# Kernel tuning notes

Hardware: AMD Instinct MI355X
Metric: run time of the kernel (lower is better)

## Reference

```python
import jax, jax.numpy as jnp
import numpy as np

B = 8388608  # 2^23 rows -> each [B,4] activation is 128 MB
N_LAYERS = 99


def setup_inputs() -> dict:
    key = jax.random.key(0)
    ks = jax.random.split(key, 7)
    return {
        "x": jax.random.normal(ks[0], (B, 2), dtype=jnp.float32),
        "W_in": jax.random.normal(ks[1], (2, 4), dtype=jnp.float32) * 0.5,
        "b_in": jax.random.normal(ks[2], (4,), dtype=jnp.float32) * 0.1,
        "Ws": jax.random.normal(ks[3], (N_LAYERS, 4, 4), dtype=jnp.float32) * 0.5,
        "bs": jax.random.normal(ks[4], (N_LAYERS, 4), dtype=jnp.float32) * 0.1,
        "W_out": jax.random.normal(ks[5], (4, 1), dtype=jnp.float32) * 0.5,
        "b_out": jax.random.normal(ks[6], (1,), dtype=jnp.float32) * 0.1,
    }


def reference(x, W_in, b_in, Ws, bs, W_out, b_out):
    # input layer + relu
    out = jax.nn.relu(x @ W_in + b_in)  # [B, 4]
    skip = out
    # torch condition `if i % 5 and i != 0` == residual whenever i % 5 != 0
    flags = (jnp.arange(N_LAYERS) % 5) != 0  # [99] bool

    def step(carry, layer):
        out, skip = carry
        W, b, flag = layer  # W: [4,4], b: [4]
        h = jax.nn.relu(out @ W + b)  # Linear(4,4) + ReLU
        new_out = jnp.where(flag, h + skip, h)
        new_skip = jnp.where(flag, new_out, skip)
        return (new_out, new_skip), None

    (out, skip), _ = jax.lax.scan(step, (out, skip), (Ws, bs, flags))
    return out @ W_out + b_out  # [B, 1]
```

## Files before the change

kernel.cpp:

```cpp
#include <hip/hip_runtime.h>


#define NLAYERS 99

__global__ __launch_bounds__(256) void skipmlp_kernel(
    const float* __restrict__ x,
    const float* __restrict__ W_in,
    const float* __restrict__ b_in,
    const float* __restrict__ Ws,
    const float* __restrict__ bs,
    const float* __restrict__ W_out,
    const float* __restrict__ b_out,
    float* __restrict__ out,
    int B)
{
    int row = blockIdx.x * blockDim.x + threadIdx.x;
    if (row >= B) return;

    const float2 xv = *reinterpret_cast<const float2*>(x + (size_t)row * 2u);

    float o0 = fmaxf(fmaf(xv.x, W_in[0], fmaf(xv.y, W_in[4], b_in[0])), 0.f);
    float o1 = fmaxf(fmaf(xv.x, W_in[1], fmaf(xv.y, W_in[5], b_in[1])), 0.f);
    float o2 = fmaxf(fmaf(xv.x, W_in[2], fmaf(xv.y, W_in[6], b_in[2])), 0.f);
    float o3 = fmaxf(fmaf(xv.x, W_in[3], fmaf(xv.y, W_in[7], b_in[3])), 0.f);

    float s0 = o0, s1 = o1, s2 = o2, s3 = o3;

    #pragma unroll 5
    for (int i = 0; i < NLAYERS; ++i) {
        const float* __restrict__ W = Ws + i * 16;
        const float* __restrict__ b = bs + i * 4;

        float h0 = fmaf(o0, W[ 0], fmaf(o1, W[ 4], fmaf(o2, W[ 8], fmaf(o3, W[12], b[0]))));
        float h1 = fmaf(o0, W[ 1], fmaf(o1, W[ 5], fmaf(o2, W[ 9], fmaf(o3, W[13], b[1]))));
        float h2 = fmaf(o0, W[ 2], fmaf(o1, W[ 6], fmaf(o2, W[10], fmaf(o3, W[14], b[2]))));
        float h3 = fmaf(o0, W[ 3], fmaf(o1, W[ 7], fmaf(o2, W[11], fmaf(o3, W[15], b[3]))));
        h0 = fmaxf(h0, 0.f);
        h1 = fmaxf(h1, 0.f);
        h2 = fmaxf(h2, 0.f);
        h3 = fmaxf(h3, 0.f);

        if ((i % 5) != 0) {
            o0 = h0 + s0; o1 = h1 + s1; o2 = h2 + s2; o3 = h3 + s3;
            s0 = o0; s1 = o1; s2 = o2; s3 = o3;
        } else {
            o0 = h0; o1 = h1; o2 = h2; o3 = h3;
        }
    }

    float y = fmaf(o0, W_out[0], fmaf(o1, W_out[1], fmaf(o2, W_out[2], fmaf(o3, W_out[3], b_out[0]))));
    out[row] = y;
}

extern "C" void kernel_launch(void* const* d_in, const int* in_sizes, int n_in,
                              void* d_out, int out_size, void* d_ws, size_t ws_size,
                              hipStream_t stream) {
    const float* x     = (const float*)d_in[0];
    const float* W_in  = (const float*)d_in[1];
    const float* b_in  = (const float*)d_in[2];
    const float* Ws    = (const float*)d_in[3];
    const float* bs    = (const float*)d_in[4];
    const float* W_out = (const float*)d_in[5];
    const float* b_out = (const float*)d_in[6];
    float* out = (float*)d_out;

    const int B = in_sizes[0] / 2;
    const int block = 256;
    const int grid = (B + block - 1) / block;

    skipmlp_kernel<<<grid, block, 0, stream>>>(x, W_in, b_in, Ws, bs, W_out, b_out, out, B);
}
```

Baseline: 570.8 us.

## Process two rows per thread with packed FP32 FMA on duplicated weights

Each thread now handles two rows and keeps the activations as float2 pairs. The layer matmuls and residual adds use the v_pk_fma_f32 and v_pk_add_f32 inline-asm instructions, so each packed instruction does the work of two scalar ones. The aim is to roughly halve the VALU instruction count in this compute-bound loop. A small prep kernel duplicates weights and biases into float2 pairs in the workspace so they can serve as the scalar-register operand. In exchange the code depends on the compiler keeping those uniform float2 values in SGPR pairs, the ReLUs stay unpacked, and it assumes B is even.

After: 569.7 us. About the same (-0.2%).

```diff
diff --git a/kernel.cpp b/kernel.cpp
--- a/kernel.cpp
+++ b/kernel.cpp
@@ -3,53 +3,81 @@
 
 #define NLAYERS 99
 
-__global__ __launch_bounds__(256) void skipmlp_kernel(
+__global__ void prep_dup_kernel(const float* __restrict__ Ws,
+                                const float* __restrict__ bs,
+                                float2* __restrict__ ws) {
+    int i = blockIdx.x * blockDim.x + threadIdx.x;
+    if (i < NLAYERS * 16) ws[i] = make_float2(Ws[i], Ws[i]);
+    if (i < NLAYERS * 4)  ws[NLAYERS * 16 + i] = make_float2(bs[i], bs[i]);
+}
+
+#define PK_FMA(h, o, w) \
+    asm("v_pk_fma_f32 %0, %1, %2, %0" : "+v"(h) : "v"(o), "s"(w))
+#define PK_ADD(d, a, b_) \
+    asm("v_pk_add_f32 %0, %1, %2" : "=v"(d) : "v"(a), "v"(b_))
+
+__global__ __launch_bounds__(256) void skipmlp_pk_kernel(
     const float* __restrict__ x,
     const float* __restrict__ W_in,
     const float* __restrict__ b_in,
-    const float* __restrict__ Ws,
-    const float* __restrict__ bs,
+    const float2* __restrict__ W2,
     const float* __restrict__ W_out,
     const float* __restrict__ b_out,
     float* __restrict__ out,
-    int B)
+    int B2)
 {
-    int row = blockIdx.x * blockDim.x + threadIdx.x;
-    if (row >= B) return;
+    int t = blockIdx.x * blockDim.x + threadIdx.x;
+    if (t >= B2) return;
 
-    const float2 xv = *reinterpret_cast<const float2*>(x + (size_t)row * 2u);
+    const float2* __restrict__ b2 = W2 + NLAYERS * 16;
 
-    float o0 = fmaxf(fmaf(xv.x, W_in[0], fmaf(xv.y, W_in[4], b_in[0])), 0.f);
-    float o1 = fmaxf(fmaf(xv.x, W_in[1], fmaf(xv.y, W_in[5], b_in[1])), 0.f);
-    float o2 = fmaxf(fmaf(xv.x, W_in[2], fmaf(xv.y, W_in[6], b_in[2])), 0.f);
-    float o3 = fmaxf(fmaf(xv.x, W_in[3], fmaf(xv.y, W_in[7], b_in[3])), 0.f);
+    const float4 xv = *reinterpret_cast<const float4*>(x + (size_t)t * 4u);
 
-    float s0 = o0, s1 = o1, s2 = o2, s3 = o3;
+    float oA0 = fmaxf(fmaf(xv.x, W_in[0], fmaf(xv.y, W_in[4], b_in[0])), 0.f);
+    float oA1 = fmaxf(fmaf(xv.x, W_in[1], fmaf(xv.y, W_in[5], b_in[1])), 0.f);
+    float oA2 = fmaxf(fmaf(xv.x, W_in[2], fmaf(xv.y, W_in[6], b_in[2])), 0.f);
+    float oA3 = fmaxf(fmaf(xv.x, W_in[3], fmaf(xv.y, W_in[7], b_in[3])), 0.f);
+    float oB0 = fmaxf(fmaf(xv.z, W_in[0], fmaf(xv.w, W_in[4], b_in[0])), 0.f);
+    float oB1 = fmaxf(fmaf(xv.z, W_in[1], fmaf(xv.w, W_in[5], b_in[1])), 0.f);
+    float oB2 = fmaxf(fmaf(xv.z, W_in[2], fmaf(xv.w, W_in[6], b_in[2])), 0.f);
+    float oB3 = fmaxf(fmaf(xv.z, W_in[3], fmaf(xv.w, W_in[7], b_in[3])), 0.f);
+
+    float2 o0 = make_float2(oA0, oB0);
+    float2 o1 = make_float2(oA1, oB1);
+    float2 o2 = make_float2(oA2, oB2);
+    float2 o3 = make_float2(oA3, oB3);
+    float2 s0 = o0, s1 = o1, s2 = o2, s3 = o3;
 
     #pragma unroll 5
     for (int i = 0; i < NLAYERS; ++i) {
-        const float* __restrict__ W = Ws + i * 16;
-        const float* __restrict__ b = bs + i * 4;
+        const float2* __restrict__ W = W2 + i * 16;
 
-        float h0 = fmaf(o0, W[ 0], fmaf(o1, W[ 4], fmaf(o2, W[ 8], fmaf(o3, W[12], b[0]))));
-        float h1 = fmaf(o0, W[ 1], fmaf(o1, W[ 5], fmaf(o2, W[ 9], fmaf(o3, W[13], b[1]))));
-        float h2 = fmaf(o0, W[ 2], fmaf(o1, W[ 6], fmaf(o2, W[10], fmaf(o3, W[14], b[2]))));
-        float h3 = fmaf(o0, W[ 3], fmaf(o1, W[ 7], fmaf(o2, W[11], fmaf(o3, W[15], b[3]))));
-        h0 = fmaxf(h0, 0.f);
-        h1 = fmaxf(h1, 0.f);
-        h2 = fmaxf(h2, 0.f);
-        h3 = fmaxf(h3, 0.f);
+        float2 h0 = b2[i * 4 + 0];
+        float2 h1 = b2[i * 4 + 1];
+        float2 h2 = b2[i * 4 + 2];
+        float2 h3 = b2[i * 4 + 3];
+
+        PK_FMA(h0, o0, W[ 0]); PK_FMA(h1, o0, W[ 1]); PK_FMA(h2, o0, W[ 2]); PK_FMA(h3, o0, W[ 3]);
+        PK_FMA(h0, o1, W[ 4]); PK_FMA(h1, o1, W[ 5]); PK_FMA(h2, o1, W[ 6]); PK_FMA(h3, o1, W[ 7]);
+        PK_FMA(h0, o2, W[ 8]); PK_FMA(h1, o2, W[ 9]); PK_FMA(h2, o2, W[10]); PK_FMA(h3, o2, W[11]);
+        PK_FMA(h0, o3, W[12]); PK_FMA(h1, o3, W[13]); PK_FMA(h2, o3, W[14]); PK_FMA(h3, o3, W[15]);
+
+        h0.x = fmaxf(h0.x, 0.f); h0.y = fmaxf(h0.y, 0.f);
+        h1.x = fmaxf(h1.x, 0.f); h1.y = fmaxf(h1.y, 0.f);
+        h2.x = fmaxf(h2.x, 0.f); h2.y = fmaxf(h2.y, 0.f);
+        h3.x = fmaxf(h3.x, 0.f); h3.y = fmaxf(h3.y, 0.f);
 
         if ((i % 5) != 0) {
-            o0 = h0 + s0; o1 = h1 + s1; o2 = h2 + s2; o3 = h3 + s3;
+            PK_ADD(o0, h0, s0); PK_ADD(o1, h1, s1); PK_ADD(o2, h2, s2); PK_ADD(o3, h3, s3);
             s0 = o0; s1 = o1; s2 = o2; s3 = o3;
         } else {
             o0 = h0; o1 = h1; o2 = h2; o3 = h3;
         }
     }
 
-    float y = fmaf(o0, W_out[0], fmaf(o1, W_out[1], fmaf(o2, W_out[2], fmaf(o3, W_out[3], b_out[0]))));
-    out[row] = y;
+    float yA = fmaf(o0.x, W_out[0], fmaf(o1.x, W_out[1], fmaf(o2.x, W_out[2], fmaf(o3.x, W_out[3], b_out[0]))));
+    float yB = fmaf(o0.y, W_out[0], fmaf(o1.y, W_out[1], fmaf(o2.y, W_out[2], fmaf(o3.y, W_out[3], b_out[0]))));
+    *reinterpret_cast<float2*>(out + (size_t)t * 2u) = make_float2(yA, yB);
 }
 
 extern "C" void kernel_launch(void* const* d_in, const int* in_sizes, int n_in,
@@ -63,10 +91,14 @@
     const float* W_out = (const float*)d_in[5];
     const float* b_out = (const float*)d_in[6];
     float* out = (float*)d_out;
+    float2* ws = (float2*)d_ws;
 
     const int B = in_sizes[0] / 2;
+    const int B2 = B / 2;
+
+    prep_dup_kernel<<<(NLAYERS * 16 + 255) / 256, 256, 0, stream>>>(Ws, bs, ws);
+
     const int block = 256;
-    const int grid = (B + block - 1) / block;
-
-    skipmlp_kernel<<<grid, block, 0, stream>>>(x, W_in, b_in, Ws, bs, W_out, b_out, out, B);
+    const int grid = (B2 + block - 1) / block;
+    skipmlp_pk_kernel<<<grid, block, 0, stream>>>(x, W_in, b_in, ws, W_out, b_out, out, B2);
 }
```

## Stage layer weights in LDS, fold skip into ReLU, prefetch next layer

Applied to the files above, without the earlier changes.

Each block copies all layer weights and biases into shared memory as float4 entries and reads them back with vector LDS loads. It prefetches the next layer's coefficients while computing the current one. The residual step is rewritten algebraically as max(Wx+b+s, s), which removes a separate add. The cost is a per-block cooperative load plus a barrier, and the scalar/constant-cache weight loads it replaces were likely already cheap, so gains depend on whether the old kernel was bound on scalar loads or latency.

New measurement: 539.4 us. -5.5%, faster.

```diff
diff --git a/kernel.cpp b/kernel.cpp
--- a/kernel.cpp
+++ b/kernel.cpp
@@ -14,6 +14,17 @@
     float* __restrict__ out,
     int B)
 {
+    __shared__ float4 lw[NLAYERS * 5];
+
+    const float4* __restrict__ Ws4 = reinterpret_cast<const float4*>(Ws);
+    const float4* __restrict__ bs4 = reinterpret_cast<const float4*>(bs);
+    for (int j4 = threadIdx.x; j4 < NLAYERS * 5; j4 += 256) {
+        int layer = j4 / 5;
+        int q = j4 - layer * 5;
+        lw[j4] = (q < 4) ? Ws4[layer * 4 + q] : bs4[layer];
+    }
+    __syncthreads();
+
     int row = blockIdx.x * blockDim.x + threadIdx.x;
     if (row >= B) return;
 
@@ -26,29 +37,43 @@
 
     float s0 = o0, s1 = o1, s2 = o2, s3 = o3;
 
-    #pragma unroll 5
-    for (int i = 0; i < NLAYERS; ++i) {
-        const float* __restrict__ W = Ws + i * 16;
-        const float* __restrict__ b = bs + i * 4;
+    float4 c0 = lw[0], c1 = lw[1], c2 = lw[2], c3 = lw[3], cb = lw[4];
 
-        float h0 = fmaf(o0, W[ 0], fmaf(o1, W[ 4], fmaf(o2, W[ 8], fmaf(o3, W[12], b[0]))));
-        float h1 = fmaf(o0, W[ 1], fmaf(o1, W[ 5], fmaf(o2, W[ 9], fmaf(o3, W[13], b[1]))));
-        float h2 = fmaf(o0, W[ 2], fmaf(o1, W[ 6], fmaf(o2, W[10], fmaf(o3, W[14], b[2]))));
-        float h3 = fmaf(o0, W[ 3], fmaf(o1, W[ 7], fmaf(o2, W[11], fmaf(o3, W[15], b[3]))));
-        h0 = fmaxf(h0, 0.f);
-        h1 = fmaxf(h1, 0.f);
-        h2 = fmaxf(h2, 0.f);
-        h3 = fmaxf(h3, 0.f);
-
-        if ((i % 5) != 0) {
-            o0 = h0 + s0; o1 = h1 + s1; o2 = h2 + s2; o3 = h3 + s3;
-            s0 = o0; s1 = o1; s2 = o2; s3 = o3;
-        } else {
-            o0 = h0; o1 = h1; o2 = h2; o3 = h3;
-        }
+#define STEP(RES, NEXT) {                                                     \
+        float4 n0 = lw[(NEXT)*5+0], n1 = lw[(NEXT)*5+1], n2 = lw[(NEXT)*5+2], \
+               n3 = lw[(NEXT)*5+3], nb = lw[(NEXT)*5+4];                      \
+        float i0, i1, i2, i3;                                                 \
+        if (RES) { i0 = cb.x + s0; i1 = cb.y + s1; i2 = cb.z + s2; i3 = cb.w + s3; } \
+        else     { i0 = cb.x;      i1 = cb.y;      i2 = cb.z;      i3 = cb.w; }      \
+        float p0 = fmaf(o0, c0.x, fmaf(o1, c1.x, fmaf(o2, c2.x, fmaf(o3, c3.x, i0)))); \
+        float p1 = fmaf(o0, c0.y, fmaf(o1, c1.y, fmaf(o2, c2.y, fmaf(o3, c3.y, i1)))); \
+        float p2 = fmaf(o0, c0.z, fmaf(o1, c1.z, fmaf(o2, c2.z, fmaf(o3, c3.z, i2)))); \
+        float p3 = fmaf(o0, c0.w, fmaf(o1, c1.w, fmaf(o2, c2.w, fmaf(o3, c3.w, i3)))); \
+        if (RES) {                                                            \
+            o0 = fmaxf(p0, s0); o1 = fmaxf(p1, s1);                           \
+            o2 = fmaxf(p2, s2); o3 = fmaxf(p3, s3);                           \
+            s0 = o0; s1 = o1; s2 = o2; s3 = o3;                               \
+        } else {                                                              \
+            o0 = fmaxf(p0, 0.f); o1 = fmaxf(p1, 0.f);                         \
+            o2 = fmaxf(p2, 0.f); o3 = fmaxf(p3, 0.f);                         \
+        }                                                                     \
+        c0 = n0; c1 = n1; c2 = n2; c3 = n3; cb = nb;                          \
     }
 
-    float y = fmaf(o0, W_out[0], fmaf(o1, W_out[1], fmaf(o2, W_out[2], fmaf(o3, W_out[3], b_out[0]))));
+    for (int base = 0; base < 95; base += 5) {
+        STEP(false, base + 1);
+        STEP(true,  base + 2);
+        STEP(true,  base + 3);
+        STEP(true,  base + 4);
+        STEP(true,  base + 5);
+    }
+    STEP(false, 96);
+    STEP(true,  97);
+    STEP(true,  98);
+    STEP(true,  98);
+#undef STEP
+
+    float y = fmaf(o0, W_out[0], fmaf(o1, W_out[1], fmaf(o2, W_out[2], o3 * W_out[3]))) + b_out[0];
     out[row] = y;
 }
 
```
